# Optimization experiments

Measured on AMD Instinct MI355X. Metric: run time of the kernel, lower is better.

## Reference

```python
import jax, jax.numpy as jnp
import numpy as np

D = 1280      # emb_dim
H = 4         # n_heads
DH = D // H
FF = 256      # dim_feedforward / hidden_dim
NL = 2        # n_layers
B = 64        # number of graphs
N = 32768     # total tokens
L = 640       # max padded length (>= max graph size w.h.p.)
EPS = 1e-5


def setup_inputs() -> dict:
    key = jax.random.key(0)
    ks = jax.random.split(key, 24)
    s = 0.02
    x = jax.random.normal(ks[0], (N, D), jnp.float32)
    batch = jnp.sort(jax.random.randint(ks[1], (N,), 0, B))
    p = {
        "x": x, "batch": batch,
        # stacked per-layer transformer params (torch Linear convention: y = x @ W.T + b)
        "Wqkv": jax.random.normal(ks[2], (NL, 3 * D, D), jnp.float32) * s,
        "bqkv": jnp.zeros((NL, 3 * D), jnp.float32),
        "Wo":   jax.random.normal(ks[3], (NL, D, D), jnp.float32) * s,
        "bo":   jnp.zeros((NL, D), jnp.float32),
        "ln1w": jnp.ones((NL, D), jnp.float32),
        "ln1b": jnp.zeros((NL, D), jnp.float32),
        "W1":   jax.random.normal(ks[4], (NL, FF, D), jnp.float32) * s,
        "b1":   jnp.zeros((NL, FF), jnp.float32),
        "W2":   jax.random.normal(ks[5], (NL, D, FF), jnp.float32) * s,
        "b2":   jnp.zeros((NL, D), jnp.float32),
        "ln2w": jnp.ones((NL, D), jnp.float32),
        "ln2b": jnp.zeros((NL, D), jnp.float32),
        # final MLP: Linear(D,FF) -> ReLU -> Linear(FF,D)
        "Wm1": jax.random.normal(ks[6], (FF, D), jnp.float32) * s,
        "bm1": jnp.zeros((FF,), jnp.float32),
        "Wm2": jax.random.normal(ks[7], (D, FF), jnp.float32) * s,
        "bm2": jnp.zeros((D,), jnp.float32),
    }
    return p


def _ln(x, w, b):
    mu = jnp.mean(x, axis=-1, keepdims=True)
    var = jnp.var(x, axis=-1, keepdims=True)
    return (x - mu) * jax.lax.rsqrt(var + EPS) * w + b


def reference(x, batch, Wqkv, bqkv, Wo, bo, ln1w, ln1b, W1, b1, W2, b2,
              ln2w, ln2b, Wm1, bm1, Wm2, bm2):
    # --- graph_to_transformer_input: scatter ragged tokens into [B, L, D] ---
    counts = jax.ops.segment_sum(jnp.ones_like(batch), batch, num_segments=B)
    offsets = jnp.concatenate([jnp.zeros((1,), counts.dtype), jnp.cumsum(counts)[:-1]])
    pos = jnp.arange(N) - offsets[batch]                 # position within each graph
    padded = jnp.zeros((B, L, D), x.dtype).at[batch, pos].set(x)
    pad_mask = jnp.arange(L)[None, :] >= counts[:, None]  # True = padding key

    h = padded
    scale = 1.0 / np.sqrt(DH)
    for l in range(NL):  # post-norm TransformerEncoderLayer, relu, dropout=eval
        qkv = h @ Wqkv[l].T + bqkv[l]
        q, k, v = jnp.split(qkv, 3, axis=-1)
        sh = lambda t: t.reshape(B, L, H, DH).transpose(0, 2, 1, 3)  # [B,H,L,DH]
        q, k, v = sh(q), sh(k), sh(v)
        scores = jnp.einsum('bhqd,bhkd->bhqk', q, k) * scale
        scores = jnp.where(pad_mask[:, None, None, :], -1e9, scores)
        attn = jax.nn.softmax(scores, axis=-1)
        o = jnp.einsum('bhqk,bhkd->bhqd', attn, v).transpose(0, 2, 1, 3).reshape(B, L, D)
        o = o @ Wo[l].T + bo[l]
        h = _ln(h + o, ln1w[l], ln1b[l])
        ff = jax.nn.relu(h @ W1[l].T + b1[l]) @ W2[l].T + b2[l]
        h = _ln(h + ff, ln2w[l], ln2b[l])

    forces = jax.nn.relu(h @ Wm1.T + bm1) @ Wm2.T + bm2   # [B, L, D]
    return forces[batch, pos]                              # gather valid tokens -> [N, D]
```

## Files before the change

kernel.cpp:

```cpp
#include <hip/hip_runtime.h>

typedef unsigned short u16;
typedef __attribute__((ext_vector_type(8))) short bf16x8;
typedef __attribute__((ext_vector_type(4))) float f32x4;

#define N_TOK 32768
#define DIM   1280
#define NH    4
#define DH    320
#define FFD   256
#define NLAYER 2
#define NB    64
#define TD    3840
#define KVD   2560

#define GLD16(gp, lp) __builtin_amdgcn_global_load_lds( \
    (const __attribute__((address_space(1))) unsigned int*)(const void*)(gp), \
    (__attribute__((address_space(3))) unsigned int*)(void*)(lp), 16, 0, 0)

__device__ __forceinline__ float b2f(u16 v) {
    union { unsigned u; float f; } c; c.u = ((unsigned)v) << 16; return c.f;
}
__device__ __forceinline__ u16 f2b(float f) {
    union { float f; unsigned u; } c; c.f = f;
    unsigned r = c.u + 0x7fffu + ((c.u >> 16) & 1u);
    return (u16)(r >> 16);
}

__global__ __launch_bounds__(256) void k_f32_to_bf16(
    const float* __restrict__ in, u16* __restrict__ out, long n)
{
    long i = ((long)blockIdx.x * 256 + threadIdx.x) * 4;
    if (i >= n) return;
    float4 v = *(const float4*)&in[i];
    ushort4 o; o.x = f2b(v.x); o.y = f2b(v.y); o.z = f2b(v.z); o.w = f2b(v.w);
    *(ushort4*)&out[i] = o;
}

__global__ void k_offsets(const int* __restrict__ batch, int* __restrict__ offs) {
    int b = threadIdx.x;
    if (b > NB) return;
    int lo = 0, hi = N_TOK;
    while (lo < hi) {
        int mid = (lo + hi) >> 1;
        if (batch[mid] < b) lo = mid + 1; else hi = mid;
    }
    offs[b] = lo;
}

__global__ __launch_bounds__(256) void k_gemm_mfma(
    const u16* __restrict__ A, int lda,
    const u16* __restrict__ W,
    const float* __restrict__ bias,
    void* __restrict__ Cv, int ldc,
    int K, int relu, int store_f32)
{
    __shared__ u16 Asm[128 * 64];
    __shared__ u16 Bsm[128 * 64];
    const int t    = threadIdx.x;
    const int lane = t & 63;
    const int w    = t >> 6;
    const int wr   = w >> 1, wc = w & 1;
    const long mBase = (long)blockIdx.y * 128;
    const long nBase = (long)blockIdx.x * 128;
    const int srow = lane >> 3;
    const int scol = (lane & 7) * 8;

    f32x4 acc[4][4];
    #pragma unroll
    for (int m = 0; m < 4; ++m)
        #pragma unroll
        for (int n = 0; n < 4; ++n) acc[m][n] = (f32x4){0.f, 0.f, 0.f, 0.f};

    for (int k0 = 0; k0 < K; k0 += 64) {
        __syncthreads();
        #pragma unroll
        for (int i = 0; i < 4; ++i) {
            const int c = w * 4 + i;
            const u16* ga = &A[(mBase + c * 8 + srow) * (long)lda + k0 + scol];
            const u16* gb = &W[(nBase + c * 8 + srow) * (long)K   + k0 + scol];
            GLD16(ga, &Asm[c * 512]);
            GLD16(gb, &Bsm[c * 512]);
        }
        __syncthreads();
        #pragma unroll
        for (int kk = 0; kk < 2; ++kk) {
            const int kc = kk * 32 + (lane >> 4) * 8;
            bf16x8 af[4], bfr[4];
            #pragma unroll
            for (int m = 0; m < 4; ++m)
                af[m] = *(const bf16x8*)&Asm[(wr * 64 + m * 16 + (lane & 15)) * 64 + kc];
            #pragma unroll
            for (int n = 0; n < 4; ++n)
                bfr[n] = *(const bf16x8*)&Bsm[(wc * 64 + n * 16 + (lane & 15)) * 64 + kc];
            #pragma unroll
            for (int m = 0; m < 4; ++m)
                #pragma unroll
                for (int n = 0; n < 4; ++n)
                    acc[m][n] = __builtin_amdgcn_mfma_f32_16x16x32_bf16(
                        af[m], bfr[n], acc[m][n], 0, 0, 0);
        }
    }

    const int ccol  = lane & 15;
    const int crow0 = (lane >> 4) * 4;
    #pragma unroll
    for (int m = 0; m < 4; ++m) {
        #pragma unroll
        for (int n = 0; n < 4; ++n) {
            const long col = nBase + wc * 64 + n * 16 + ccol;
            const float bv = bias[col];
            #pragma unroll
            for (int r = 0; r < 4; ++r) {
                const long row = mBase + wr * 64 + m * 16 + crow0 + r;
                float v = acc[m][n][r] + bv;
                if (relu) v = fmaxf(v, 0.f);
                if (store_f32) ((float*)Cv)[row * (long)ldc + col] = v;
                else           ((u16*)Cv)[row * (long)ldc + col] = f2b(v);
            }
        }
    }
}

__global__ __launch_bounds__(256) void k_ln_residual(
    const u16* __restrict__ a, const u16* __restrict__ delta,
    const float* __restrict__ w, const float* __restrict__ bb,
    u16* __restrict__ out)
{
    const long row = blockIdx.x;
    const int t = threadIdx.x;
    float v[5];
    float s = 0.f, s2 = 0.f;
    #pragma unroll
    for (int k = 0; k < 5; ++k) {
        int c = t + (k << 8);
        float xv = b2f(a[row * DIM + c]) + b2f(delta[row * DIM + c]);
        v[k] = xv; s += xv; s2 += xv * xv;
    }
    #pragma unroll
    for (int off = 32; off > 0; off >>= 1) {
        s  += __shfl_down(s, off);
        s2 += __shfl_down(s2, off);
    }
    __shared__ float red[8];
    __shared__ float stat[2];
    const int wid = t >> 6;
    if ((t & 63) == 0) { red[wid] = s; red[wid + 4] = s2; }
    __syncthreads();
    if (t == 0) {
        float S  = red[0] + red[1] + red[2] + red[3];
        float S2 = red[4] + red[5] + red[6] + red[7];
        float mu  = S * (1.f / DIM);
        float var = S2 * (1.f / DIM) - mu * mu;
        stat[0] = mu;
        stat[1] = rsqrtf(fmaxf(var, 0.f) + 1e-5f);
    }
    __syncthreads();
    float mu = stat[0], inv = stat[1];
    #pragma unroll
    for (int k = 0; k < 5; ++k) {
        int c = t + (k << 8);
        out[row * DIM + c] = f2b((v[k] - mu) * inv * w[c] + bb[c]);
    }
}

__global__ __launch_bounds__(256) void k_attn_mfma(
    u16* __restrict__ q, const u16* __restrict__ kv, const int* __restrict__ offs)
{
    __shared__ u16 KV[11520];
    __shared__ float Ssm[32 * 33];
    __shared__ u16 Plds[32 * 40];
    __shared__ float mL[32], lL[32], aL[32];

    const int lin = blockIdx.x;
    const int gLo = lin & 7;
    const int j   = lin >> 3;
    const int g   = (j / 80) * 8 + gLo;
    const int rem = j % 80;
    const int hh  = rem / 20;
    const int qt  = rem % 20;

    const int gstart = offs[g];
    const int n = offs[g + 1] - gstart;
    if (qt * 32 >= n) return;
    const int nq = min(32, n - qt * 32);
    const int t    = threadIdx.x;
    const int lane = t & 63;
    const int w    = t >> 6;
    const int qr   = w >> 1, kr = w & 1;
    const int l15  = lane & 15;
    const int l4   = lane >> 4;
    const float scale = 0.05590169943749474f;

    if (t < 32) { mL[t] = -1e30f; lL[t] = 0.f; }

    bf16x8 qf[10];
    {
        int qrl = qt * 32 + qr * 16 + l15;
        if (qrl >= n) qrl = n - 1;
        const u16* gq = &q[(long)(gstart + qrl) * DIM + hh * DH + l4 * 8];
        #pragma unroll
        for (int c = 0; c < 10; ++c)
            qf[c] = *(const bf16x8*)&gq[c * 32];
    }

    f32x4 oacc[2][5];
    #pragma unroll
    for (int a = 0; a < 2; ++a)
        #pragma unroll
        for (int f = 0; f < 5; ++f) oacc[a][f] = (f32x4){0.f, 0.f, 0.f, 0.f};

    const int spos = t >> 3;
    const int sfb  = (t & 7) * 40;
    const int vpp  = t & 15;
    const int vfb  = (t >> 4) * 20;

    for (int kb = 0; kb < n; kb += 32) {
        const int nk = min(32, n - kb);
        __syncthreads();

        {
            int gp = kb + spos; if (gp >= n) gp = n - 1;
            const u16* gk = &kv[(long)(gstart + gp) * KVD + hh * DH + sfb];
            uint4 c0 = *(const uint4*)(gk + 0);
            uint4 c1 = *(const uint4*)(gk + 8);
            uint4 c2 = *(const uint4*)(gk + 16);
            uint4 c3 = *(const uint4*)(gk + 24);
            uint4 c4 = *(const uint4*)(gk + 32);
            u16* dst = &KV[spos * 328 + sfb];
            *(uint4*)(dst + 0)  = c0;
            *(uint4*)(dst + 8)  = c1;
            *(uint4*)(dst + 16) = c2;
            *(uint4*)(dst + 24) = c3;
            *(uint4*)(dst + 32) = c4;
        }
        __syncthreads();

        {
            f32x4 sacc = (f32x4){0.f, 0.f, 0.f, 0.f};
            #pragma unroll
            for (int c = 0; c < 10; ++c) {
                bf16x8 kf = *(const bf16x8*)&KV[(kr * 16 + l15) * 328 + c * 32 + l4 * 8];
                sacc = __builtin_amdgcn_mfma_f32_16x16x32_bf16(qf[c], kf, sacc, 0, 0, 0);
            }
            const int col = kr * 16 + l15;
            const int srow0 = qr * 16 + l4 * 4;
            const bool masked = (col >= nk);
            #pragma unroll
            for (int r = 0; r < 4; ++r)
                Ssm[(srow0 + r) * 33 + col] = masked ? -1e30f : sacc[r] * scale;
        }
        __syncthreads();

        {
            uint2 va4[5], vb4[5];
            int p0 = kb + 2 * vpp, p1 = p0 + 1;
            if (p0 >= n) p0 = n - 1;
            if (p1 >= n) p1 = n - 1;
            const u16* g0 = &kv[(long)(gstart + p0) * KVD + DIM + hh * DH + vfb];
            const u16* g1 = &kv[(long)(gstart + p1) * KVD + DIM + hh * DH + vfb];
            #pragma unroll
            for (int i = 0; i < 5; ++i) {
                va4[i] = *(const uint2*)(g0 + i * 4);
                vb4[i] = *(const uint2*)(g1 + i * 4);
            }

            const int r  = t >> 3;
            const int cg = (t & 7) * 4;
            float4 s4 = *(const float4*)&Ssm[r * 33 + cg];
            float mx = fmaxf(fmaxf(s4.x, s4.y), fmaxf(s4.z, s4.w));
            mx = fmaxf(mx, __shfl_xor(mx, 1));
            mx = fmaxf(mx, __shfl_xor(mx, 2));
            mx = fmaxf(mx, __shfl_xor(mx, 4));
            const float mo = mL[r];
            const float mn = fmaxf(mo, mx);
            float p0f = __expf(s4.x - mn), p1f = __expf(s4.y - mn);
            float p2f = __expf(s4.z - mn), p3f = __expf(s4.w - mn);
            union { u16 h[4]; uint2 u; } pw;
            pw.h[0] = f2b(p0f); pw.h[1] = f2b(p1f); pw.h[2] = f2b(p2f); pw.h[3] = f2b(p3f);
            *(uint2*)&Plds[r * 40 + cg] = pw.u;
            float rs = p0f + p1f + p2f + p3f;
            rs += __shfl_xor(rs, 1);
            rs += __shfl_xor(rs, 2);
            rs += __shfl_xor(rs, 4);
            if ((t & 7) == 0) {
                const float al = __expf(mo - mn);
                aL[r] = al;
                lL[r] = lL[r] * al + rs;
                mL[r] = mn;
            }
            #pragma unroll
            for (int i = 0; i < 5; ++i) {
                const unsigned a0 = va4[i].x, a1 = va4[i].y;
                const unsigned b0 = vb4[i].x, b1 = vb4[i].y;
                const int fb = vfb + i * 4;
                *(unsigned*)&KV[(fb + 0) * 36 + 2 * vpp] = (a0 & 0xffffu) | (b0 << 16);
                *(unsigned*)&KV[(fb + 1) * 36 + 2 * vpp] = (a0 >> 16) | (b0 & 0xffff0000u);
                *(unsigned*)&KV[(fb + 2) * 36 + 2 * vpp] = (a1 & 0xffffu) | (b1 << 16);
                *(unsigned*)&KV[(fb + 3) * 36 + 2 * vpp] = (a1 >> 16) | (b1 & 0xffff0000u);
            }
        }
        __syncthreads();

        {
            float al[2][4];
            #pragma unroll
            for (int a = 0; a < 2; ++a)
                #pragma unroll
                for (int r = 0; r < 4; ++r)
                    al[a][r] = aL[a * 16 + l4 * 4 + r];
            #pragma unroll
            for (int a = 0; a < 2; ++a)
                #pragma unroll
                for (int f = 0; f < 5; ++f)
                    #pragma unroll
                    for (int r = 0; r < 4; ++r)
                        oacc[a][f][r] *= al[a][r];
            #pragma unroll
            for (int a = 0; a < 2; ++a) {
                bf16x8 pf = *(const bf16x8*)&Plds[(a * 16 + l15) * 40 + l4 * 8];
                #pragma unroll
                for (int f = 0; f < 5; ++f) {
                    const int fe = w * 80 + f * 16 + l15;
                    union { bf16x8 v; uint2 u[2]; } uv;
                    uv.u[0] = *(const uint2*)&KV[fe * 36 + l4 * 8];
                    uv.u[1] = *(const uint2*)&KV[fe * 36 + l4 * 8 + 4];
                    oacc[a][f] = __builtin_amdgcn_mfma_f32_16x16x32_bf16(
                        pf, uv.v, oacc[a][f], 0, 0, 0);
                }
            }
        }
    }

    float invl[2][4];
    #pragma unroll
    for (int a = 0; a < 2; ++a)
        #pragma unroll
        for (int r = 0; r < 4; ++r)
            invl[a][r] = 1.f / lL[a * 16 + l4 * 4 + r];
    #pragma unroll
    for (int a = 0; a < 2; ++a) {
        #pragma unroll
        for (int f = 0; f < 5; ++f) {
            #pragma unroll
            for (int r = 0; r < 4; ++r) {
                const int lrow = a * 16 + l4 * 4 + r;
                if (lrow < nq) {
                    const long grow = (long)(gstart + qt * 32 + lrow);
                    q[grow * DIM + hh * DH + w * 80 + f * 16 + l15] =
                        f2b(oacc[a][f][r] * invl[a][r]);
                }
            }
        }
    }
}

extern "C" void kernel_launch(void* const* d_in, const int* in_sizes, int n_in,
                              void* d_out, int out_size, void* d_ws, size_t ws_size,
                              hipStream_t stream) {
    const float* x     = (const float*)d_in[0];
    const int*   batch = (const int*)d_in[1];
    const float* Wqkv  = (const float*)d_in[2];
    const float* bqkv  = (const float*)d_in[3];
    const float* Wo    = (const float*)d_in[4];
    const float* bo    = (const float*)d_in[5];
    const float* ln1w  = (const float*)d_in[6];
    const float* ln1b  = (const float*)d_in[7];
    const float* W1    = (const float*)d_in[8];
    const float* b1    = (const float*)d_in[9];
    const float* W2    = (const float*)d_in[10];
    const float* b2    = (const float*)d_in[11];
    const float* ln2w  = (const float*)d_in[12];
    const float* ln2b  = (const float*)d_in[13];
    const float* Wm1   = (const float*)d_in[14];
    const float* bm1   = (const float*)d_in[15];
    const float* Wm2   = (const float*)d_in[16];
    const float* bm2   = (const float*)d_in[17];

    float* outF = (float*)d_out;
    u16*   qbuf = (u16*)d_out;

    char* ws   = (char*)d_ws;
    int*  offs = (int*)ws;
    u16*  h    = (u16*)(ws + 1024);
    u16*  kvb  = h + (size_t)N_TOK * DIM;
    u16*  tmp  = kvb;
    u16*  ff   = kvb + (size_t)N_TOK * DIM;
    u16*  wqkv_bf = kvb + (size_t)N_TOK * KVD;
    u16*  wo_bf   = wqkv_bf + (size_t)NLAYER * TD * DIM;
    u16*  w1_bf   = wo_bf   + (size_t)NLAYER * DIM * DIM;
    u16*  w2_bf   = w1_bf   + (size_t)NLAYER * FFD * DIM;
    u16*  wm1_bf  = w2_bf   + (size_t)NLAYER * DIM * FFD;
    u16*  wm2_bf  = wm1_bf  + (size_t)FFD * DIM;

    k_offsets<<<1, 128, 0, stream>>>(batch, offs);
    {
        long n = (long)N_TOK * DIM;
        k_f32_to_bf16<<<(int)(n / 1024), 256, 0, stream>>>(x, h, n);
        long nqkv = (long)NLAYER * TD * DIM;
        k_f32_to_bf16<<<(int)(nqkv / 1024), 256, 0, stream>>>(Wqkv, wqkv_bf, nqkv);
        long nwo = (long)NLAYER * DIM * DIM;
        k_f32_to_bf16<<<(int)(nwo / 1024), 256, 0, stream>>>(Wo, wo_bf, nwo);
        long nw1 = (long)NLAYER * FFD * DIM;
        k_f32_to_bf16<<<(int)(nw1 / 1024), 256, 0, stream>>>(W1, w1_bf, nw1);
        long nw2 = (long)NLAYER * DIM * FFD;
        k_f32_to_bf16<<<(int)(nw2 / 1024), 256, 0, stream>>>(W2, w2_bf, nw2);
        long nm = (long)FFD * DIM;
        k_f32_to_bf16<<<(int)(nm / 1024), 256, 0, stream>>>(Wm1, wm1_bf, nm);
        k_f32_to_bf16<<<(int)(nm / 1024), 256, 0, stream>>>(Wm2, wm2_bf, nm);
    }

    dim3 blk(256);
    for (int l = 0; l < NLAYER; ++l) {
        const u16*   Wl = wqkv_bf + (size_t)l * TD * DIM;
        const float* bl = bqkv + (size_t)l * TD;
        k_gemm_mfma<<<dim3(DIM / 128, N_TOK / 128), blk, 0, stream>>>(
            h, DIM, Wl, bl, qbuf, DIM, DIM, 0, 0);
        k_gemm_mfma<<<dim3(KVD / 128, N_TOK / 128), blk, 0, stream>>>(
            h, DIM, Wl + (size_t)DIM * DIM, bl + DIM, kvb, KVD, DIM, 0, 0);
        k_attn_mfma<<<dim3(20 * NH * NB), blk, 0, stream>>>(qbuf, kvb, offs);
        k_gemm_mfma<<<dim3(DIM / 128, N_TOK / 128), blk, 0, stream>>>(
            qbuf, DIM, wo_bf + (size_t)l * DIM * DIM, bo + (size_t)l * DIM,
            tmp, DIM, DIM, 0, 0);
        k_ln_residual<<<N_TOK, blk, 0, stream>>>(
            h, tmp, ln1w + (size_t)l * DIM, ln1b + (size_t)l * DIM, h);
        k_gemm_mfma<<<dim3(FFD / 128, N_TOK / 128), blk, 0, stream>>>(
            h, DIM, w1_bf + (size_t)l * FFD * DIM, b1 + (size_t)l * FFD,
            ff, FFD, DIM, 1, 0);
        k_gemm_mfma<<<dim3(DIM / 128, N_TOK / 128), blk, 0, stream>>>(
            ff, FFD, w2_bf + (size_t)l * DIM * FFD, b2 + (size_t)l * DIM,
            tmp, DIM, FFD, 0, 0);
        k_ln_residual<<<N_TOK, blk, 0, stream>>>(
            h, tmp, ln2w + (size_t)l * DIM, ln2b + (size_t)l * DIM, h);
    }
    k_gemm_mfma<<<dim3(FFD / 128, N_TOK / 128), blk, 0, stream>>>(
        h, DIM, wm1_bf, bm1, ff, FFD, DIM, 1, 0);
    k_gemm_mfma<<<dim3(DIM / 128, N_TOK / 128), blk, 0, stream>>>(
        ff, FFD, wm2_bf, bm2, outF, DIM, FFD, 0, 1);
}
```

Measured before the change: 2.845 ms.

## Fuse QKV GEMMs, merge weight conversions, read K directly in attention

Three changes land together. The six weight-conversion launches become one kernel that branches on the element index, and the separate Q and KV projection GEMMs become one QKV GEMM that routes output columns to the Q or KV buffer. The attention kernel now loads K fragments straight from global memory into registers instead of staging them in LDS, which removes one barrier per key block, and it adds s_setprio around the MFMA loops. The direct K loads rely on cache hits in place of LDS reuse across waves, and an extra barrier is added at the end of each loop iteration.

```diff
diff --git a/kernel.cpp b/kernel.cpp
--- a/kernel.cpp
+++ b/kernel.cpp
@@ -35,6 +35,33 @@
     float4 v = *(const float4*)&in[i];
     ushort4 o; o.x = f2b(v.x); o.y = f2b(v.y); o.z = f2b(v.z); o.w = f2b(v.w);
     *(ushort4*)&out[i] = o;
+}
+
+#define E0 9830400L
+#define E1 13107200L
+#define E2 13762560L
+#define E3 14417920L
+#define E4 14745600L
+#define E5 15073280L
+__global__ __launch_bounds__(256) void k_conv_weights(
+    const float* __restrict__ Wqkv, const float* __restrict__ Wo,
+    const float* __restrict__ W1,   const float* __restrict__ W2,
+    const float* __restrict__ Wm1,  const float* __restrict__ Wm2,
+    u16* __restrict__ d0, u16* __restrict__ d1, u16* __restrict__ d2,
+    u16* __restrict__ d3, u16* __restrict__ d4, u16* __restrict__ d5)
+{
+    long i = ((long)blockIdx.x * 256 + threadIdx.x) * 4;
+    if (i >= E5) return;
+    const float* src; u16* dst; long off;
+    if      (i < E0) { src = Wqkv; dst = d0; off = i; }
+    else if (i < E1) { src = Wo;   dst = d1; off = i - E0; }
+    else if (i < E2) { src = W1;   dst = d2; off = i - E1; }
+    else if (i < E3) { src = W2;   dst = d3; off = i - E2; }
+    else if (i < E4) { src = Wm1;  dst = d4; off = i - E3; }
+    else             { src = Wm2;  dst = d5; off = i - E4; }
+    float4 v = *(const float4*)&src[off];
+    ushort4 o; o.x = f2b(v.x); o.y = f2b(v.y); o.z = f2b(v.z); o.w = f2b(v.w);
+    *(ushort4*)&dst[off] = o;
 }
 
 __global__ void k_offsets(const int* __restrict__ batch, int* __restrict__ offs) {
@@ -122,6 +149,79 @@
     }
 }
 
+__global__ __launch_bounds__(256) void k_gemm_qkv(
+    const u16* __restrict__ A,
+    const u16* __restrict__ W,
+    const float* __restrict__ bias,
+    u16* __restrict__ qd, u16* __restrict__ kvd)
+{
+    __shared__ u16 Asm[128 * 64];
+    __shared__ u16 Bsm[128 * 64];
+    const int t    = threadIdx.x;
+    const int lane = t & 63;
+    const int w    = t >> 6;
+    const int wr   = w >> 1, wc = w & 1;
+    const long mBase = (long)blockIdx.y * 128;
+    const long nBase = (long)blockIdx.x * 128;
+    const int srow = lane >> 3;
+    const int scol = (lane & 7) * 8;
+
+    f32x4 acc[4][4];
+    #pragma unroll
+    for (int m = 0; m < 4; ++m)
+        #pragma unroll
+        for (int n = 0; n < 4; ++n) acc[m][n] = (f32x4){0.f, 0.f, 0.f, 0.f};
+
+    for (int k0 = 0; k0 < DIM; k0 += 64) {
+        __syncthreads();
+        #pragma unroll
+        for (int i = 0; i < 4; ++i) {
+            const int c = w * 4 + i;
+            const u16* ga = &A[(mBase + c * 8 + srow) * (long)DIM + k0 + scol];
+            const u16* gb = &W[(nBase + c * 8 + srow) * (long)DIM + k0 + scol];
+            GLD16(ga, &Asm[c * 512]);
+            GLD16(gb, &Bsm[c * 512]);
+        }
+        __syncthreads();
+        #pragma unroll
+        for (int kk = 0; kk < 2; ++kk) {
+            const int kc = kk * 32 + (lane >> 4) * 8;
+            bf16x8 af[4], bfr[4];
+            #pragma unroll
+            for (int m = 0; m < 4; ++m)
+                af[m] = *(const bf16x8*)&Asm[(wr * 64 + m * 16 + (lane & 15)) * 64 + kc];
+            #pragma unroll
+            for (int n = 0; n < 4; ++n)
+                bfr[n] = *(const bf16x8*)&Bsm[(wc * 64 + n * 16 + (lane & 15)) * 64 + kc];
+            #pragma unroll
+            for (int m = 0; m < 4; ++m)
+                #pragma unroll
+                for (int n = 0; n < 4; ++n)
+                    acc[m][n] = __builtin_amdgcn_mfma_f32_16x16x32_bf16(
+                        af[m], bfr[n], acc[m][n], 0, 0, 0);
+        }
+    }
+
+    const int ccol  = lane & 15;
+    const int crow0 = (lane >> 4) * 4;
+    const bool isQ = (nBase < DIM);
+    #pragma unroll
+    for (int m = 0; m < 4; ++m) {
+        #pragma unroll
+        for (int n = 0; n < 4; ++n) {
+            const long col = nBase + wc * 64 + n * 16 + ccol;
+            const float bv = bias[col];
+            #pragma unroll
+            for (int r = 0; r < 4; ++r) {
+                const long row = mBase + wr * 64 + m * 16 + crow0 + r;
+                float v = acc[m][n][r] + bv;
+                if (isQ) qd[row * (long)DIM + col]          = f2b(v);
+                else     kvd[row * (long)KVD + (col - DIM)] = f2b(v);
+            }
+        }
+    }
+}
+
 __global__ __launch_bounds__(256) void k_ln_residual(
     const u16* __restrict__ a, const u16* __restrict__ delta,
     const float* __restrict__ w, const float* __restrict__ bb,
@@ -167,7 +267,7 @@
 __global__ __launch_bounds__(256) void k_attn_mfma(
     u16* __restrict__ q, const u16* __restrict__ kv, const int* __restrict__ offs)
 {
-    __shared__ u16 KV[11520];
+    __shared__ u16 Vt[320 * 36];
     __shared__ float Ssm[32 * 33];
     __shared__ u16 Plds[32 * 40];
     __shared__ float mL[32], lL[32], aL[32];
@@ -210,50 +310,14 @@
         #pragma unroll
         for (int f = 0; f < 5; ++f) oacc[a][f] = (f32x4){0.f, 0.f, 0.f, 0.f};
 
-    const int spos = t >> 3;
-    const int sfb  = (t & 7) * 40;
     const int vpp  = t & 15;
     const int vfb  = (t >> 4) * 20;
 
     for (int kb = 0; kb < n; kb += 32) {
         const int nk = min(32, n - kb);
-        __syncthreads();
-
+
+        uint2 va4[5], vb4[5];
         {
-            int gp = kb + spos; if (gp >= n) gp = n - 1;
-            const u16* gk = &kv[(long)(gstart + gp) * KVD + hh * DH + sfb];
-            uint4 c0 = *(const uint4*)(gk + 0);
-            uint4 c1 = *(const uint4*)(gk + 8);
-            uint4 c2 = *(const uint4*)(gk + 16);
-            uint4 c3 = *(const uint4*)(gk + 24);
-            uint4 c4 = *(const uint4*)(gk + 32);
-            u16* dst = &KV[spos * 328 + sfb];
-            *(uint4*)(dst + 0)  = c0;
-            *(uint4*)(dst + 8)  = c1;
-            *(uint4*)(dst + 16) = c2;
-            *(uint4*)(dst + 24) = c3;
-            *(uint4*)(dst + 32) = c4;
-        }
-        __syncthreads();
-
-        {
-            f32x4 sacc = (f32x4){0.f, 0.f, 0.f, 0.f};
-            #pragma unroll
-            for (int c = 0; c < 10; ++c) {
-                bf16x8 kf = *(const bf16x8*)&KV[(kr * 16 + l15) * 328 + c * 32 + l4 * 8];
-                sacc = __builtin_amdgcn_mfma_f32_16x16x32_bf16(qf[c], kf, sacc, 0, 0, 0);
-            }
-            const int col = kr * 16 + l15;
-            const int srow0 = qr * 16 + l4 * 4;
-            const bool masked = (col >= nk);
-            #pragma unroll
-            for (int r = 0; r < 4; ++r)
-                Ssm[(srow0 + r) * 33 + col] = masked ? -1e30f : sacc[r] * scale;
-        }
-        __syncthreads();
-
-        {
-            uint2 va4[5], vb4[5];
             int p0 = kb + 2 * vpp, p1 = p0 + 1;
             if (p0 >= n) p0 = n - 1;
             if (p1 >= n) p1 = n - 1;
@@ -264,7 +328,30 @@
                 va4[i] = *(const uint2*)(g0 + i * 4);
                 vb4[i] = *(const uint2*)(g1 + i * 4);
             }
-
+        }
+
+        {
+            int krow = kb + kr * 16 + l15;
+            if (krow >= n) krow = n - 1;
+            const u16* gk = &kv[(long)(gstart + krow) * KVD + hh * DH + l4 * 8];
+            f32x4 sacc = (f32x4){0.f, 0.f, 0.f, 0.f};
+            __builtin_amdgcn_s_setprio(1);
+            #pragma unroll
+            for (int c = 0; c < 10; ++c) {
+                bf16x8 kf = *(const bf16x8*)&gk[c * 32];
+                sacc = __builtin_amdgcn_mfma_f32_16x16x32_bf16(qf[c], kf, sacc, 0, 0, 0);
+            }
+            __builtin_amdgcn_s_setprio(0);
+            const int col = kr * 16 + l15;
+            const int srow0 = qr * 16 + l4 * 4;
+            const bool masked = (col >= nk);
+            #pragma unroll
+            for (int r = 0; r < 4; ++r)
+                Ssm[(srow0 + r) * 33 + col] = masked ? -1e30f : sacc[r] * scale;
+        }
+        __syncthreads();
+
+        {
             const int r  = t >> 3;
             const int cg = (t & 7) * 4;
             float4 s4 = *(const float4*)&Ssm[r * 33 + cg];
@@ -294,10 +381,10 @@
                 const unsigned a0 = va4[i].x, a1 = va4[i].y;
                 const unsigned b0 = vb4[i].x, b1 = vb4[i].y;
                 const int fb = vfb + i * 4;
-                *(unsigned*)&KV[(fb + 0) * 36 + 2 * vpp] = (a0 & 0xffffu) | (b0 << 16);
-                *(unsigned*)&KV[(fb + 1) * 36 + 2 * vpp] = (a0 >> 16) | (b0 & 0xffff0000u);
-                *(unsigned*)&KV[(fb + 2) * 36 + 2 * vpp] = (a1 & 0xffffu) | (b1 << 16);
-                *(unsigned*)&KV[(fb + 3) * 36 + 2 * vpp] = (a1 >> 16) | (b1 & 0xffff0000u);
+                *(unsigned*)&Vt[(fb + 0) * 36 + 2 * vpp] = (a0 & 0xffffu) | (b0 << 16);
+                *(unsigned*)&Vt[(fb + 1) * 36 + 2 * vpp] = (a0 >> 16) | (b0 & 0xffff0000u);
+                *(unsigned*)&Vt[(fb + 2) * 36 + 2 * vpp] = (a1 & 0xffffu) | (b1 << 16);
+                *(unsigned*)&Vt[(fb + 3) * 36 + 2 * vpp] = (a1 >> 16) | (b1 & 0xffff0000u);
             }
         }
         __syncthreads();
@@ -316,6 +403,7 @@
                     #pragma unroll
                     for (int r = 0; r < 4; ++r)
                         oacc[a][f][r] *= al[a][r];
+            __builtin_amdgcn_s_setprio(1);
             #pragma unroll
             for (int a = 0; a < 2; ++a) {
                 bf16x8 pf = *(const bf16x8*)&Plds[(a * 16 + l15) * 40 + l4 * 8];
@@ -323,13 +411,15 @@
                 for (int f = 0; f < 5; ++f) {
                     const int fe = w * 80 + f * 16 + l15;
                     union { bf16x8 v; uint2 u[2]; } uv;
-                    uv.u[0] = *(const uint2*)&KV[fe * 36 + l4 * 8];
-                    uv.u[1] = *(const uint2*)&KV[fe * 36 + l4 * 8 + 4];
+                    uv.u[0] = *(const uint2*)&Vt[fe * 36 + l4 * 8];
+                    uv.u[1] = *(const uint2*)&Vt[fe * 36 + l4 * 8 + 4];
                     oacc[a][f] = __builtin_amdgcn_mfma_f32_16x16x32_bf16(
                         pf, uv.v, oacc[a][f], 0, 0, 0);
                 }
             }
-        }
+            __builtin_amdgcn_s_setprio(0);
+        }
+        __syncthreads();
     }
 
     float invl[2][4];
@@ -397,27 +487,17 @@
     {
         long n = (long)N_TOK * DIM;
         k_f32_to_bf16<<<(int)(n / 1024), 256, 0, stream>>>(x, h, n);
-        long nqkv = (long)NLAYER * TD * DIM;
-        k_f32_to_bf16<<<(int)(nqkv / 1024), 256, 0, stream>>>(Wqkv, wqkv_bf, nqkv);
-        long nwo = (long)NLAYER * DIM * DIM;
-        k_f32_to_bf16<<<(int)(nwo / 1024), 256, 0, stream>>>(Wo, wo_bf, nwo);
-        long nw1 = (long)NLAYER * FFD * DIM;
-        k_f32_to_bf16<<<(int)(nw1 / 1024), 256, 0, stream>>>(W1, w1_bf, nw1);
-        long nw2 = (long)NLAYER * DIM * FFD;
-        k_f32_to_bf16<<<(int)(nw2 / 1024), 256, 0, stream>>>(W2, w2_bf, nw2);
-        long nm = (long)FFD * DIM;
-        k_f32_to_bf16<<<(int)(nm / 1024), 256, 0, stream>>>(Wm1, wm1_bf, nm);
-        k_f32_to_bf16<<<(int)(nm / 1024), 256, 0, stream>>>(Wm2, wm2_bf, nm);
+        k_conv_weights<<<(int)(E5 / 1024), 256, 0, stream>>>(
+            Wqkv, Wo, W1, W2, Wm1, Wm2,
+            wqkv_bf, wo_bf, w1_bf, w2_bf, wm1_bf, wm2_bf);
     }
 
     dim3 blk(256);
     for (int l = 0; l < NLAYER; ++l) {
         const u16*   Wl = wqkv_bf + (size_t)l * TD * DIM;
         const float* bl = bqkv + (size_t)l * TD;
-        k_gemm_mfma<<<dim3(DIM / 128, N_TOK / 128), blk, 0, stream>>>(
-            h, DIM, Wl, bl, qbuf, DIM, DIM, 0, 0);
-        k_gemm_mfma<<<dim3(KVD / 128, N_TOK / 128), blk, 0, stream>>>(
-            h, DIM, Wl + (size_t)DIM * DIM, bl + DIM, kvb, KVD, DIM, 0, 0);
+        k_gemm_qkv<<<dim3(TD / 128, N_TOK / 128), blk, 0, stream>>>(
+            h, Wl, bl, qbuf, kvb);
         k_attn_mfma<<<dim3(20 * NH * NB), blk, 0, stream>>>(qbuf, kvb, offs);
         k_gemm_mfma<<<dim3(DIM / 128, N_TOK / 128), blk, 0, stream>>>(
             qbuf, DIM, wo_bf + (size_t)l * DIM * DIM, bo + (size_t)l * DIM,
```

Measured after the change: 3.244 ms. +14.0%, slower.
